# Kernel tuning notes

Hardware: AMD Instinct MI355X
Metric: run time of the kernel (lower is better)

Reference implementation:

```python
import jax, jax.numpy as jnp
import numpy as np

LEAK = 0.01
EPS = 1e-5


def _gcn(x, W, b, src, dst, n):
    # GCNConv: add self-loops, symmetric D^-1/2 (A+I) D^-1/2 normalization
    h = x @ W
    loop = jnp.arange(n)
    s = jnp.concatenate([src, loop])
    d = jnp.concatenate([dst, loop])
    deg = jax.ops.segment_sum(jnp.ones(s.shape[0], h.dtype), d, num_segments=n)
    dinv = jnp.where(deg > 0, jax.lax.rsqrt(deg), 0.0)
    norm = dinv[s] * dinv[d]
    out = jax.ops.segment_sum(h[s] * norm[:, None], d, num_segments=n)
    return out + b


def _sage(x, Wl, bl, Wr, src, dst, n):
    # SAGEConv (mean aggr): lin_l(mean_neigh) + lin_r(x); bias on lin_l
    cnt = jax.ops.segment_sum(jnp.ones(src.shape[0], x.dtype), dst, num_segments=n)
    agg = jax.ops.segment_sum(x[src], dst, num_segments=n) / jnp.maximum(cnt, 1.0)[:, None]
    return agg @ Wl + bl + x @ Wr


def _bn(x, g, b):
    # BatchNorm over node dim, batch statistics (training forward), biased var
    m = x.mean(0)
    v = jnp.mean((x - m) ** 2, axis=0)
    return (x - m) * jax.lax.rsqrt(v + EPS) * g + b


def _lrelu(x):
    return jnp.where(x >= 0, x, LEAK * x)


def setup_inputs() -> dict:
    key = jax.random.key(0)
    ks = jax.random.split(key, 20)
    N, E, F_IN, H, G, L = 50000, 800000, 128, 128, 1000, 1000
    h2, h4, OUT = H // 2, H // 4, 32
    x = jax.random.normal(ks[0], (N, F_IN), dtype=jnp.float32)
    edge_index = jax.random.randint(ks[1], (2, E), 0, N)
    batch = jnp.sort(jax.random.randint(ks[2], (N,), 0, G))
    link_indices = jax.random.randint(ks[3], (2, L), 0, G)
    s = 0.05
    return {
        "x": x, "edge_index": edge_index, "batch": batch,
        "link_indices": link_indices, "num_graphs": G,
        "W1": jax.random.normal(ks[4], (F_IN, H), jnp.float32) * s,
        "b1": jnp.zeros((H,), jnp.float32),
        "g1": jnp.ones((H,), jnp.float32), "be1": jnp.zeros((H,), jnp.float32),
        "Wl2": jax.random.normal(ks[5], (H, h2), jnp.float32) * s,
        "bl2": jnp.zeros((h2,), jnp.float32),
        "Wr2": jax.random.normal(ks[6], (H, h2), jnp.float32) * s,
        "g2": jnp.ones((h2,), jnp.float32), "be2": jnp.zeros((h2,), jnp.float32),
        "W3": jax.random.normal(ks[7], (h2, h4), jnp.float32) * s,
        "b3": jnp.zeros((h4,), jnp.float32),
        "g3": jnp.ones((h4,), jnp.float32), "be3": jnp.zeros((h4,), jnp.float32),
        "W4": jax.random.normal(ks[8], (h4, OUT), jnp.float32) * s,
        "b4": jnp.zeros((OUT,), jnp.float32),
    }


def reference(x, edge_index, batch, link_indices, num_graphs,
              W1, b1, g1, be1, Wl2, bl2, Wr2, g2, be2,
              W3, b3, g3, be3, W4, b4):
    n = x.shape[0]
    src, dst = edge_index[0], edge_index[1]
    h = _lrelu(_bn(_gcn(x, W1, b1, src, dst, n), g1, be1))        # dropout = identity (eval)
    h = _lrelu(_bn(_sage(h, Wl2, bl2, Wr2, src, dst, n), g2, be2))
    h = _lrelu(_bn(_gcn(h, W3, b3, src, dst, n), g3, be3))
    h = _gcn(h, W4, b4, src, dst, n)
    g = jax.ops.segment_sum(h, batch, num_segments=num_graphs)     # global_add_pool
    src_emb = g[link_indices[0]]
    tgt_emb = g[link_indices[1]]
    return jax.nn.sigmoid(jnp.sum(src_emb * tgt_emb, axis=1))
```

## Files before the change

### kernel.cpp

```cpp
#include <hip/hip_runtime.h>
#include <math.h>

#define LEAK 0.01f
#define BNEPS 1e-5f
#define NCH 256
#define NGMAX 1024
#define NSLOT 64

typedef __attribute__((ext_vector_type(8))) short bf16x8;
typedef __attribute__((ext_vector_type(4))) float f32x4;
typedef __attribute__((ext_vector_type(2))) float f32x2;

__device__ inline unsigned bfpack(float a, float b) {
  unsigned ua = __float_as_uint(a);
  unsigned ub = __float_as_uint(b);
  unsigned ra = (ua + 0x7fffu + ((ua >> 16) & 1u)) >> 16;
  unsigned rb = (ub + 0x7fffu + ((ub >> 16) & 1u)) & 0xffff0000u;
  return ra | rb;
}
__device__ inline unsigned short bfround(float a) {
  unsigned ua = __float_as_uint(a);
  return (unsigned short)((ua + 0x7fffu + ((ua >> 16) & 1u)) >> 16);
}
__device__ inline float2 bfunpack(unsigned u) {
  float2 r;
  r.x = __uint_as_float(u << 16);
  r.y = __uint_as_float(u & 0xffff0000u);
  return r;
}
__device__ inline unsigned char f32_to_fp8(float v) {
  int p = __builtin_amdgcn_cvt_pk_fp8_f32(v, v, 0, false);
  return (unsigned char)(p & 0xff);
}

__global__ __launch_bounds__(256) void k_hist(const int* __restrict__ dst,
                                              int* __restrict__ H, int E, int NBK) {
  __shared__ int h[256];
  h[threadIdx.x] = 0;
  __syncthreads();
  int chunk = (E + NCH - 1) / NCH;
  int lo = blockIdx.x * chunk, hi = min(lo + chunk, E);
  for (int e = lo + threadIdx.x; e < hi; e += 256)
    atomicAdd(&h[dst[e] >> 8], 1);
  __syncthreads();
  if (threadIdx.x < NBK) H[threadIdx.x * NCH + blockIdx.x] = h[threadIdx.x];
}

__global__ __launch_bounds__(256) void k_gscan1(const int* __restrict__ in,
                                                int* __restrict__ bsum, int m) {
  int i = blockIdx.x * 256 + threadIdx.x;
  int v = (i < m) ? in[i] : 0;
#pragma unroll
  for (int s = 1; s < 64; s <<= 1) v += __shfl_xor(v, s, 64);
  __shared__ int ws[4];
  if ((threadIdx.x & 63) == 0) ws[threadIdx.x >> 6] = v;
  __syncthreads();
  if (threadIdx.x == 0) bsum[blockIdx.x] = ws[0] + ws[1] + ws[2] + ws[3];
}
__global__ __launch_bounds__(256) void k_gscan2(int* __restrict__ bsum, int NB) {
  __shared__ int lds[256];
  int t = threadIdx.x;
  int v = (t < NB) ? bsum[t] : 0;
  lds[t] = v;
  __syncthreads();
  for (int ofs = 1; ofs < 256; ofs <<= 1) {
    int u = (t >= ofs) ? lds[t - ofs] : 0;
    __syncthreads();
    lds[t] += u;
    __syncthreads();
  }
  if (t < NB) bsum[t] = lds[t] - v;
}
__global__ __launch_bounds__(256) void k_gscan3(const int* __restrict__ in,
                                                const int* __restrict__ boff,
                                                int* __restrict__ out, int m) {
  __shared__ int lds[256];
  int t = threadIdx.x;
  int i = blockIdx.x * 256 + t;
  int v = (i < m) ? in[i] : 0;
  lds[t] = v;
  __syncthreads();
  for (int ofs = 1; ofs < 256; ofs <<= 1) {
    int u = (t >= ofs) ? lds[t - ofs] : 0;
    __syncthreads();
    lds[t] += u;
    __syncthreads();
  }
  if (i < m) out[i] = boff[blockIdx.x] + lds[t] - v;
}

__global__ __launch_bounds__(256) void k_scatter_bkt(
    const int* __restrict__ src, const int* __restrict__ dst,
    const int* __restrict__ O, int* __restrict__ ebuf, int E, int NBK) {
  __shared__ int cur[256];
  if (threadIdx.x < NBK) cur[threadIdx.x] = O[threadIdx.x * NCH + blockIdx.x];
  __syncthreads();
  int chunk = (E + NCH - 1) / NCH;
  int lo = blockIdx.x * chunk, hi = min(lo + chunk, E);
  for (int e = lo + threadIdx.x; e < hi; e += 256) {
    int d = dst[e];
    int pos = atomicAdd(&cur[d >> 8], 1);
    ebuf[pos] = src[e] | ((d & 255) << 24);
  }
}

__global__ __launch_bounds__(256) void k_fill2(
    const int* __restrict__ ebuf, const int* __restrict__ O,
    int* __restrict__ eidx, int* __restrict__ rowptr,
    float* __restrict__ dinv, float* __restrict__ invcnt,
    int E, int n, int NBK) {
  __shared__ int hist[256];
  __shared__ int sc[256];
  __shared__ int cur[256];
  const int b = blockIdx.x;
  const int t = threadIdx.x;
  const int lo = O[b * NCH];
  const int hi = (b + 1 < NBK) ? O[(b + 1) * NCH] : E;
  hist[t] = 0;
  __syncthreads();
  for (int e = lo + t; e < hi; e += 256)
    atomicAdd(&hist[(ebuf[e] >> 24) & 255], 1);
  __syncthreads();
  int v = hist[t];
  sc[t] = v;
  __syncthreads();
  for (int ofs = 1; ofs < 256; ofs <<= 1) {
    int u = (t >= ofs) ? sc[t - ofs] : 0;
    __syncthreads();
    sc[t] += u;
    __syncthreads();
  }
  int excl = sc[t] - v;
  cur[t] = lo + excl;
  int node = b * 256 + t;
  if (node < n) {
    rowptr[node] = lo + excl;
    float d = (float)v;
    dinv[node]   = rsqrtf(d + 1.0f);
    invcnt[node] = 1.0f / fmaxf(d, 1.0f);
  }
  if (node == n || (b == NBK - 1 && t == 255)) rowptr[n] = E;
  __syncthreads();
  for (int e = lo + t; e < hi; e += 256) {
    int p = ebuf[e];
    int pos = atomicAdd(&cur[(p >> 24) & 255], 1);
    eidx[pos] = p & 0xFFFFFF;
  }
}

template<int F, bool FP8, bool GCN, bool ADD, bool STATS, bool POOL>
__global__ __launch_bounds__(256) void k_gather(
    const void* __restrict__ Hn, const unsigned short* __restrict__ Hbf,
    const float* __restrict__ scale,
    const int* __restrict__ rowptr, const int* __restrict__ eidx,
    const float* __restrict__ bias, const float* __restrict__ addf,
    unsigned short* __restrict__ outb,
    float* __restrict__ partials, const int* __restrict__ batch,
    float* __restrict__ gpool, int n) {
  constexpr int COLS = F / 8;
  constexpr int EPI  = 64 / COLS;
  const int wid  = threadIdx.x >> 6;
  const int v    = blockIdx.x * 4 + wid;
  const bool valid = v < n;
  const int lane = threadIdx.x & 63;
  const int col  = lane % COLS;
  const int eo   = lane / COLS;

  const int lo = valid ? rowptr[v] : 0;
  const int hi = valid ? rowptr[v + 1] : 0;
  float a[8] = {0.f,0.f,0.f,0.f,0.f,0.f,0.f,0.f};
  int myE = (lo + lane < hi) ? eidx[lo + lane] : 0;
  for (int base = lo; base < hi; base += 64) {
    int cnt = min(hi - base, 64);
    int nxt = (base + 64 + lane < hi) ? eidx[base + 64 + lane] : 0;
#pragma unroll 4
    for (int t = eo; t < cnt; t += EPI) {
      int s = __shfl(myE, t, 64);
      if constexpr (FP8) {
        uint2 q = *(const uint2*)((const unsigned char*)Hn + (long long)s * F + col * 8);
        f32x2 p0 = __builtin_amdgcn_cvt_pk_f32_fp8(q.x, false);
        f32x2 p1 = __builtin_amdgcn_cvt_pk_f32_fp8(q.x, true);
        f32x2 p2 = __builtin_amdgcn_cvt_pk_f32_fp8(q.y, false);
        f32x2 p3 = __builtin_amdgcn_cvt_pk_f32_fp8(q.y, true);
        a[0]+=p0[0]; a[1]+=p0[1]; a[2]+=p1[0]; a[3]+=p1[1];
        a[4]+=p2[0]; a[5]+=p2[1]; a[6]+=p3[0]; a[7]+=p3[1];
      } else {
        uint4 hv = *(const uint4*)((const unsigned short*)Hn + (long long)s * F + col * 8);
        float2 p0 = bfunpack(hv.x), p1 = bfunpack(hv.y);
        float2 p2 = bfunpack(hv.z), p3 = bfunpack(hv.w);
        a[0]+=p0.x; a[1]+=p0.y; a[2]+=p1.x; a[3]+=p1.y;
        a[4]+=p2.x; a[5]+=p2.y; a[6]+=p3.x; a[7]+=p3.y;
      }
    }
    myE = nxt;
  }
#pragma unroll
  for (int m = COLS; m < 64; m <<= 1) {
#pragma unroll
    for (int j = 0; j < 8; j++) a[j] += __shfl_xor(a[j], m, 64);
  }

  float o[8] = {0.f,0.f,0.f,0.f,0.f,0.f,0.f,0.f};
  if (eo == 0 && valid) {
    float sv = scale[v];
    if constexpr (GCN) {
      uint4 hv = *(const uint4*)&Hbf[(long long)v * F + col * 8];
      float2 p0 = bfunpack(hv.x), p1 = bfunpack(hv.y);
      float2 p2 = bfunpack(hv.z), p3 = bfunpack(hv.w);
      float h[8] = {p0.x,p0.y,p1.x,p1.y,p2.x,p2.y,p3.x,p3.y};
#pragma unroll
      for (int j = 0; j < 8; j++) o[j] = bias[col * 8 + j] + sv * (a[j] + h[j]);
    } else if constexpr (ADD) {
      const float4 t0 = *(const float4*)&addf[(long long)v * F + col * 8];
      const float4 t1 = *(const float4*)&addf[(long long)v * F + col * 8 + 4];
      o[0]=fmaf(sv,a[0],t0.x); o[1]=fmaf(sv,a[1],t0.y);
      o[2]=fmaf(sv,a[2],t0.z); o[3]=fmaf(sv,a[3],t0.w);
      o[4]=fmaf(sv,a[4],t1.x); o[5]=fmaf(sv,a[5],t1.y);
      o[6]=fmaf(sv,a[6],t1.z); o[7]=fmaf(sv,a[7],t1.w);
    } else {
#pragma unroll
      for (int j = 0; j < 8; j++) o[j] = sv * a[j];
    }
    if constexpr (POOL) {
      int g = batch[v];
#pragma unroll
      for (int j = 0; j < 8; j++) atomicAdd(&gpool[(long long)g * F + col * 8 + j], o[j]);
    } else {
      uint4 u;
      u.x = bfpack(o[0], o[1]); u.y = bfpack(o[2], o[3]);
      u.z = bfpack(o[4], o[5]); u.w = bfpack(o[6], o[7]);
      *(uint4*)&outb[(long long)v * F + col * 8] = u;
    }
  }

  if constexpr (STATS) {
    __shared__ float sred[4][2 * F];
    if (eo == 0) {
#pragma unroll
      for (int j = 0; j < 8; j++) {
        sred[wid][col * 8 + j]     = o[j];
        sred[wid][F + col * 8 + j] = o[j] * o[j];
      }
    }
    __syncthreads();
    int t = threadIdx.x;
    if (t < 2 * F) {
      float s = sred[0][t] + sred[1][t] + sred[2][t] + sred[3][t];
      atomicAdd(&partials[(blockIdx.x & (NSLOT - 1)) * 2 * F + t], s);
    }
  }
}

template<int K, int F, bool XBF, bool BNIN, bool F8OUT>
__global__ __launch_bounds__(256) void k_gemm_mfma(
    const void* __restrict__ Xv, const float* __restrict__ W,
    const float* __restrict__ pin, const float* __restrict__ gw,
    const float* __restrict__ bw, float invN,
    const float* __restrict__ prescale,
    unsigned short* __restrict__ Yb, unsigned char* __restrict__ Yf8,
    float* __restrict__ zptr, int zcnt, int n) {
  constexpr int SP  = K + 8;
  constexpr int NCT = F / 16;
  __shared__ unsigned short sX[64 * SP];
  __shared__ unsigned short sWT[F * SP];
  __shared__ float sbn[BNIN ? 2 * K : 1];

  for (int i = blockIdx.x * 256 + threadIdx.x; i < zcnt; i += gridDim.x * 256)
    zptr[i] = 0.f;

  const int row0 = blockIdx.x * 64;
  if constexpr (BNIN) {
    int t = threadIdx.x;
    if (t < K) {
      float s1 = 0.f, s2 = 0.f;
      for (int s = 0; s < NSLOT; s++) {
        s1 += pin[s * 2 * K + t];
        s2 += pin[s * 2 * K + K + t];
      }
      float m   = s1 * invN;
      float var = s2 * invN - m * m;
      float scv = gw[t] * rsqrtf(var + BNEPS);
      sbn[t]     = scv;
      sbn[K + t] = bw[t] - m * scv;
    }
    __syncthreads();
  }
  for (int i = threadIdx.x; i < (K / 2) * F; i += 256) {
    int nn = i % F;
    int kk = (i / F) * 2;
    float w0 = W[(long long)kk * F + nn];
    float w1 = W[(long long)(kk + 1) * F + nn];
    *(unsigned*)&sWT[nn * SP + kk] = bfpack(w0, w1);
  }
  for (int i = threadIdx.x; i < 64 * (K / 8); i += 256) {
    int r = i / (K / 8), k8 = (i % (K / 8)) * 8;
    int gr = row0 + r;
    uint4 u = {0, 0, 0, 0};
    if (gr < n) {
      if constexpr (XBF) {
        const unsigned short* X = (const unsigned short*)Xv;
        uint4 raw = *(const uint4*)&X[(long long)gr * K + k8];
        if constexpr (BNIN) {
          float2 p0 = bfunpack(raw.x), p1 = bfunpack(raw.y);
          float2 p2 = bfunpack(raw.z), p3 = bfunpack(raw.w);
          float y[8] = {p0.x,p0.y,p1.x,p1.y,p2.x,p2.y,p3.x,p3.y};
#pragma unroll
          for (int j = 0; j < 8; j++) {
            float t = fmaf(y[j], sbn[k8 + j], sbn[K + k8 + j]);
            y[j] = (t >= 0.f) ? t : LEAK * t;
          }
          u.x = bfpack(y[0], y[1]); u.y = bfpack(y[2], y[3]);
          u.z = bfpack(y[4], y[5]); u.w = bfpack(y[6], y[7]);
        } else {
          u = raw;
        }
      } else {
        const float* X = (const float*)Xv;
        float4 xa = *(const float4*)&X[(long long)gr * K + k8];
        float4 xb = *(const float4*)&X[(long long)gr * K + k8 + 4];
        u.x = bfpack(xa.x, xa.y); u.y = bfpack(xa.z, xa.w);
        u.z = bfpack(xb.x, xb.y); u.w = bfpack(xb.z, xb.w);
      }
    }
    *(uint4*)&sX[r * SP + k8] = u;
  }
  __syncthreads();

  const int wv   = threadIdx.x >> 6;
  const int lane = threadIdx.x & 63;
  const int l16  = lane & 15;
  const int quad = lane >> 4;
  f32x4 acc[NCT];
#pragma unroll
  for (int c = 0; c < NCT; c++) acc[c] = (f32x4){0.f, 0.f, 0.f, 0.f};

#pragma unroll
  for (int k0 = 0; k0 < K; k0 += 32) {
    bf16x8 af = *(const bf16x8*)&sX[(wv * 16 + l16) * SP + k0 + quad * 8];
#pragma unroll
    for (int c = 0; c < NCT; c++) {
      bf16x8 bfr = *(const bf16x8*)&sWT[(c * 16 + l16) * SP + k0 + quad * 8];
      acc[c] = __builtin_amdgcn_mfma_f32_16x16x32_bf16(af, bfr, acc[c], 0, 0, 0);
    }
  }

  const int rbase = row0 + wv * 16 + quad * 4;
  float ps[4];
#pragma unroll
  for (int rg = 0; rg < 4; rg++) {
    int gr = rbase + rg;
    ps[rg] = (prescale && gr < n) ? prescale[gr] : 1.0f;
  }
#pragma unroll
  for (int c = 0; c < NCT; c++) {
    int col = c * 16 + l16;
#pragma unroll
    for (int rg = 0; rg < 4; rg++) {
      int gr = rbase + rg;
      if (gr < n) {
        float val = acc[c][rg] * ps[rg];
        Yb[(long long)gr * F + col] = bfround(val);
        if constexpr (F8OUT) Yf8[(long long)gr * F + col] = f32_to_fp8(val);
      }
    }
  }
}

__global__ __launch_bounds__(256) void k_gemm_sage_mfma(
    const unsigned short* __restrict__ X, const float* __restrict__ Wl,
    const float* __restrict__ Wr, const float* __restrict__ bl,
    const float* __restrict__ pin, const float* __restrict__ gw,
    const float* __restrict__ bw, float invN,
    unsigned char* __restrict__ t1f8, float* __restrict__ t2,
    float* __restrict__ zptr, int zcnt, int n) {
  constexpr int K = 128, F = 64, SP = K + 8, NCT = F / 16;
  __shared__ unsigned short sX[64 * SP];
  __shared__ unsigned short sWlT[F * SP];
  __shared__ unsigned short sWrT[F * SP];
  __shared__ float sbn[2 * K];

  for (int i = blockIdx.x * 256 + threadIdx.x; i < zcnt; i += gridDim.x * 256)
    zptr[i] = 0.f;

  {
    int t = threadIdx.x;
    if (t < K) {
      float s1 = 0.f, s2 = 0.f;
      for (int s = 0; s < NSLOT; s++) {
        s1 += pin[s * 2 * K + t];
        s2 += pin[s * 2 * K + K + t];
      }
      float m   = s1 * invN;
      float var = s2 * invN - m * m;
      float scv = gw[t] * rsqrtf(var + BNEPS);
      sbn[t]     = scv;
      sbn[K + t] = bw[t] - m * scv;
    }
  }
  __syncthreads();
  const int row0 = blockIdx.x * 64;
  for (int i = threadIdx.x; i < (K / 2) * F; i += 256) {
    int nn = i % F;
    int kk = (i / F) * 2;
    *(unsigned*)&sWlT[nn * SP + kk] =
        bfpack(Wl[(long long)kk * F + nn], Wl[(long long)(kk + 1) * F + nn]);
    *(unsigned*)&sWrT[nn * SP + kk] =
        bfpack(Wr[(long long)kk * F + nn], Wr[(long long)(kk + 1) * F + nn]);
  }
  for (int i = threadIdx.x; i < 64 * (K / 8); i += 256) {
    int r = i / (K / 8), k8 = (i % (K / 8)) * 8;
    int gr = row0 + r;
    uint4 u = {0, 0, 0, 0};
    if (gr < n) {
      uint4 raw = *(const uint4*)&X[(long long)gr * K + k8];
      float2 p0 = bfunpack(raw.x), p1 = bfunpack(raw.y);
      float2 p2 = bfunpack(raw.z), p3 = bfunpack(raw.w);
      float y[8] = {p0.x,p0.y,p1.x,p1.y,p2.x,p2.y,p3.x,p3.y};
#pragma unroll
      for (int j = 0; j < 8; j++) {
        float t = fmaf(y[j], sbn[k8 + j], sbn[K + k8 + j]);
        y[j] = (t >= 0.f) ? t : LEAK * t;
      }
      u.x = bfpack(y[0], y[1]); u.y = bfpack(y[2], y[3]);
      u.z = bfpack(y[4], y[5]); u.w = bfpack(y[6], y[7]);
    }
    *(uint4*)&sX[r * SP + k8] = u;
  }
  __syncthreads();

  const int wv   = threadIdx.x >> 6;
  const int lane = threadIdx.x & 63;
  const int l16  = lane & 15;
  const int quad = lane >> 4;
  f32x4 a1[NCT], a2[NCT];
#pragma unroll
  for (int c = 0; c < NCT; c++) {
    a1[c] = (f32x4){0.f, 0.f, 0.f, 0.f};
    a2[c] = (f32x4){0.f, 0.f, 0.f, 0.f};
  }
#pragma unroll
  for (int k0 = 0; k0 < K; k0 += 32) {
    bf16x8 af = *(const bf16x8*)&sX[(wv * 16 + l16) * SP + k0 + quad * 8];
#pragma unroll
    for (int c = 0; c < NCT; c++) {
      bf16x8 bl8 = *(const bf16x8*)&sWlT[(c * 16 + l16) * SP + k0 + quad * 8];
      bf16x8 br8 = *(const bf16x8*)&sWrT[(c * 16 + l16) * SP + k0 + quad * 8];
      a1[c] = __builtin_amdgcn_mfma_f32_16x16x32_bf16(af, bl8, a1[c], 0, 0, 0);
      a2[c] = __builtin_amdgcn_mfma_f32_16x16x32_bf16(af, br8, a2[c], 0, 0, 0);
    }
  }
  const int rbase = row0 + wv * 16 + quad * 4;
#pragma unroll
  for (int c = 0; c < NCT; c++) {
    int col = c * 16 + l16;
    float blv = bl[col];
#pragma unroll
    for (int rg = 0; rg < 4; rg++) {
      int gr = rbase + rg;
      if (gr < n) {
        t1f8[(long long)gr * F + col] = f32_to_fp8(a1[c][rg]);
        t2[(long long)gr * F + col]   = a2[c][rg] + blv;
      }
    }
  }
}

__global__ void k_link(const float* __restrict__ g, const int* __restrict__ li0,
                       const int* __restrict__ li1, float* __restrict__ out, int L) {
  int i = blockIdx.x * blockDim.x + threadIdx.x;
  if (i >= L) return;
  const float* a = g + (long long)li0[i] * 32;
  const float* b = g + (long long)li1[i] * 32;
  float s = 0.f;
#pragma unroll
  for (int f = 0; f < 32; f++) s = fmaf(a[f], b[f], s);
  out[i] = 1.0f / (1.0f + expf(-s));
}

extern "C" void kernel_launch(void* const* d_in, const int* in_sizes, int n_in,
                              void* d_out, int out_size, void* d_ws, size_t ws_size,
                              hipStream_t stream) {
  const float* x   = (const float*)d_in[0];
  const int* ei    = (const int*)d_in[1];
  const int* batch = (const int*)d_in[2];
  const int* li    = (const int*)d_in[3];
  const float* W1  = (const float*)d_in[5];
  const float* b1  = (const float*)d_in[6];
  const float* g1  = (const float*)d_in[7];
  const float* be1 = (const float*)d_in[8];
  const float* Wl2 = (const float*)d_in[9];
  const float* bl2 = (const float*)d_in[10];
  const float* Wr2 = (const float*)d_in[11];
  const float* g2  = (const float*)d_in[12];
  const float* be2 = (const float*)d_in[13];
  const float* W3  = (const float*)d_in[14];
  const float* b3  = (const float*)d_in[15];
  const float* g3  = (const float*)d_in[16];
  const float* be3 = (const float*)d_in[17];
  const float* W4  = (const float*)d_in[18];
  const float* b4  = (const float*)d_in[19];

  const int n = in_sizes[0] / 128;
  const int E = in_sizes[1] / 2;
  const int L = in_sizes[3] / 2;
  const int* src = ei;
  const int* dst = ei + E;
  const int* li0 = li;
  const int* li1 = li + L;
  const int NBK = (n + 255) / 256;

  char* base = (char*)d_ws;
  size_t off = 0;
  auto alloc = [&](size_t bytes) -> void* {
    void* p = (void*)(base + off);
    off = (off + bytes + 255) & ~(size_t)255;
    return p;
  };
  int*   H      = (int*)alloc((size_t)NBK * NCH * 4);
  int*   O      = (int*)alloc((size_t)NBK * NCH * 4);
  int*   hsum   = (int*)alloc((size_t)1024 * 4);
  int*   ebuf   = (int*)alloc((size_t)E * 4);
  int*   eidx   = (int*)alloc((size_t)E * 4);
  int*   rowptr = (int*)alloc((size_t)(n + 1) * 4);
  float* dinv   = (float*)alloc((size_t)n * 4);
  float* invcnt = (float*)alloc((size_t)n * 4);
  float* partials1 = (float*)alloc((size_t)NSLOT * 256 * 4);
  float* partials2 = (float*)alloc((size_t)NSLOT * 128 * 4);
  float* partials3 = (float*)alloc((size_t)NSLOT * 64 * 4);
  float* gpool  = (float*)alloc((size_t)NGMAX * 32 * 4);
  unsigned short* h1b  = (unsigned short*)alloc((size_t)n * 128 * 2);
  unsigned char*  h1f8 = (unsigned char*)alloc((size_t)n * 128);
  unsigned short* a1b  = (unsigned short*)alloc((size_t)n * 128 * 2);
  unsigned char*  t1f8 = (unsigned char*)alloc((size_t)n * 64);
  float*          t2f  = (float*)alloc((size_t)n * 64 * 4);
  unsigned short* h2b  = (unsigned short*)alloc((size_t)n * 64 * 2);
  unsigned short* h3gb = (unsigned short*)alloc((size_t)n * 32 * 2);
  unsigned short* a3b  = (unsigned short*)alloc((size_t)n * 32 * 2);
  unsigned short* h4b  = (unsigned short*)alloc((size_t)n * 32 * 2);
  (void)ws_size; (void)n_in; (void)out_size;

  const int BT = 256;
  auto cdiv = [](long long a, long long b) { return (int)((a + b - 1) / b); };
  const int GB  = cdiv(n, 4);
  const int GM  = cdiv(n, 64);
  const int MH  = NBK * NCH;
  const int NBH = cdiv(MH, 256);
  const float invN = 1.0f / (float)n;

  k_hist<<<NCH, 256, 0, stream>>>(dst, H, E, NBK);
  k_gscan1<<<NBH, 256, 0, stream>>>(H, hsum, MH);
  k_gscan2<<<1, 256, 0, stream>>>(hsum, NBH);
  k_gscan3<<<NBH, 256, 0, stream>>>(H, hsum, O, MH);
  k_scatter_bkt<<<NCH, 256, 0, stream>>>(src, dst, O, ebuf, E, NBK);
  k_fill2<<<NBK, 256, 0, stream>>>(ebuf, O, eidx, rowptr, dinv, invcnt, E, n, NBK);

  k_gemm_mfma<128,128,false,false,true><<<GM, 256, 0, stream>>>(
      x, W1, nullptr, nullptr, nullptr, 0.f, dinv, h1b, h1f8,
      partials1, NSLOT * 256, n);
  k_gather<128,true,true,false,true,false><<<GB, 256, 0, stream>>>(
      h1f8, h1b, dinv, rowptr, eidx, b1, nullptr, a1b,
      partials1, nullptr, nullptr, n);

  k_gemm_sage_mfma<<<GM, 256, 0, stream>>>(
      a1b, Wl2, Wr2, bl2, partials1, g1, be1, invN, t1f8, t2f,
      partials2, NSLOT * 128, n);
  k_gather<64,true,false,true,true,false><<<GB, 256, 0, stream>>>(
      t1f8, nullptr, invcnt, rowptr, eidx, nullptr, t2f, h2b,
      partials2, nullptr, nullptr, n);

  k_gemm_mfma<64,32,true,true,false><<<GM, 256, 0, stream>>>(
      h2b, W3, partials2, g2, be2, invN, dinv, h3gb, nullptr,
      partials3, NSLOT * 64, n);
  k_gather<32,false,true,false,true,false><<<GB, 256, 0, stream>>>(
      h3gb, h3gb, dinv, rowptr, eidx, b3, nullptr, a3b,
      partials3, nullptr, nullptr, n);

  k_gemm_mfma<32,32,true,true,false><<<GM, 256, 0, stream>>>(
      a3b, W4, partials3, g3, be3, invN, dinv, h4b, nullptr,
      gpool, NGMAX * 32, n);
  k_gather<32,false,true,false,false,true><<<GB, 256, 0, stream>>>(
      h4b, h4b, dinv, rowptr, eidx, b4, nullptr, nullptr,
      nullptr, batch, gpool, n);

  k_link<<<cdiv(L, BT), BT, 0, stream>>>(gpool, li0, li1, (float*)d_out, L);
}
```

Baseline: 357.6 us.

## Map multiple nodes per wave in gather kernels with per-lane edge batches

```diff
diff --git a/kernel.cpp b/kernel.cpp
--- a/kernel.cpp
+++ b/kernel.cpp
@@ -158,61 +158,86 @@
     float* __restrict__ partials, const int* __restrict__ batch,
     float* __restrict__ gpool, int n) {
   constexpr int COLS = F / 8;
-  constexpr int EPI  = 64 / COLS;
-  const int wid  = threadIdx.x >> 6;
-  const int v    = blockIdx.x * 4 + wid;
+  constexpr int GPW  = 64 / COLS;
+  constexpr int NPB  = 4 * GPW;
+  constexpr int K    = 16 / COLS;
+
+  const int tid  = threadIdx.x;
+  const int wave = tid >> 6;
+  const int lane = tid & 63;
+  const int l    = lane % COLS;
+  const int g    = lane / COLS;
+  const int vb   = (int)blockIdx.x * NPB;
+  const int v    = vb + wave * GPW + g;
   const bool valid = v < n;
-  const int lane = threadIdx.x & 63;
-  const int col  = lane % COLS;
-  const int eo   = lane / COLS;
+
+  __shared__ float sred[STATS ? 2 * F : 1];
+  __shared__ float pool[POOL ? NPB * 32 : 1];
+  int gbase = 0;
+  if constexpr (STATS) {
+    if (tid < 2 * F) sred[tid] = 0.f;
+  }
+  if constexpr (POOL) {
+    for (int i = tid; i < NPB * 32; i += 256) pool[i] = 0.f;
+    gbase = batch[min(vb, n - 1)];
+  }
+  if constexpr (STATS || POOL) __syncthreads();
 
   const int lo = valid ? rowptr[v] : 0;
   const int hi = valid ? rowptr[v + 1] : 0;
   float a[8] = {0.f,0.f,0.f,0.f,0.f,0.f,0.f,0.f};
-  int myE = (lo + lane < hi) ? eidx[lo + lane] : 0;
-  for (int base = lo; base < hi; base += 64) {
-    int cnt = min(hi - base, 64);
-    int nxt = (base + 64 + lane < hi) ? eidx[base + 64 + lane] : 0;
-#pragma unroll 4
-    for (int t = eo; t < cnt; t += EPI) {
-      int s = __shfl(myE, t, 64);
-      if constexpr (FP8) {
-        uint2 q = *(const uint2*)((const unsigned char*)Hn + (long long)s * F + col * 8);
-        f32x2 p0 = __builtin_amdgcn_cvt_pk_f32_fp8(q.x, false);
-        f32x2 p1 = __builtin_amdgcn_cvt_pk_f32_fp8(q.x, true);
-        f32x2 p2 = __builtin_amdgcn_cvt_pk_f32_fp8(q.y, false);
-        f32x2 p3 = __builtin_amdgcn_cvt_pk_f32_fp8(q.y, true);
-        a[0]+=p0[0]; a[1]+=p0[1]; a[2]+=p1[0]; a[3]+=p1[1];
-        a[4]+=p2[0]; a[5]+=p2[1]; a[6]+=p3[0]; a[7]+=p3[1];
-      } else {
-        uint4 hv = *(const uint4*)((const unsigned short*)Hn + (long long)s * F + col * 8);
-        float2 p0 = bfunpack(hv.x), p1 = bfunpack(hv.y);
-        float2 p2 = bfunpack(hv.z), p3 = bfunpack(hv.w);
-        a[0]+=p0.x; a[1]+=p0.y; a[2]+=p1.x; a[3]+=p1.y;
-        a[4]+=p2.x; a[5]+=p2.y; a[6]+=p3.x; a[7]+=p3.y;
-      }
-    }
-    myE = nxt;
-  }
-#pragma unroll
-  for (int m = COLS; m < 64; m <<= 1) {
-#pragma unroll
-    for (int j = 0; j < 8; j++) a[j] += __shfl_xor(a[j], m, 64);
+
+  int trips = (hi - lo + 15) >> 4;
+#pragma unroll
+  for (int m = 1; m < 64; m <<= 1) trips = max(trips, __shfl_xor(trips, m, 64));
+
+  for (int bb = 0; bb < trips; bb++) {
+    const int b = lo + bb * 16;
+    int pre[K];
+#pragma unroll
+    for (int kk = 0; kk < K; kk++) {
+      int e = b + l * K + kk;
+      pre[kk] = (e < hi) ? eidx[e] : 0;
+    }
+#pragma unroll
+    for (int j = 0; j < 16; j++) {
+      int s = __shfl(pre[j % K], g * COLS + j / K, 64);
+      if (b + j < hi) {
+        if constexpr (FP8) {
+          uint2 q = *(const uint2*)((const unsigned char*)Hn + (long long)s * F + l * 8);
+          f32x2 p0 = __builtin_amdgcn_cvt_pk_f32_fp8(q.x, false);
+          f32x2 p1 = __builtin_amdgcn_cvt_pk_f32_fp8(q.x, true);
+          f32x2 p2 = __builtin_amdgcn_cvt_pk_f32_fp8(q.y, false);
+          f32x2 p3 = __builtin_amdgcn_cvt_pk_f32_fp8(q.y, true);
+          a[0]+=p0[0]; a[1]+=p0[1]; a[2]+=p1[0]; a[3]+=p1[1];
+          a[4]+=p2[0]; a[5]+=p2[1]; a[6]+=p3[0]; a[7]+=p3[1];
+        } else {
+          uint4 hv = *(const uint4*)((const unsigned short*)Hn + (long long)s * F + l * 8);
+          float2 p0 = bfunpack(hv.x), p1 = bfunpack(hv.y);
+          float2 p2 = bfunpack(hv.z), p3 = bfunpack(hv.w);
+          a[0]+=p0.x; a[1]+=p0.y; a[2]+=p1.x; a[3]+=p1.y;
+          a[4]+=p2.x; a[5]+=p2.y; a[6]+=p3.x; a[7]+=p3.y;
+        }
+      }
+    }
   }
 
   float o[8] = {0.f,0.f,0.f,0.f,0.f,0.f,0.f,0.f};
-  if (eo == 0 && valid) {
+  if (valid) {
     float sv = scale[v];
     if constexpr (GCN) {
-      uint4 hv = *(const uint4*)&Hbf[(long long)v * F + col * 8];
+      uint4 hv = *(const uint4*)&Hbf[(long long)v * F + l * 8];
       float2 p0 = bfunpack(hv.x), p1 = bfunpack(hv.y);
       float2 p2 = bfunpack(hv.z), p3 = bfunpack(hv.w);
       float h[8] = {p0.x,p0.y,p1.x,p1.y,p2.x,p2.y,p3.x,p3.y};
-#pragma unroll
-      for (int j = 0; j < 8; j++) o[j] = bias[col * 8 + j] + sv * (a[j] + h[j]);
+      const float4 b0 = *(const float4*)&bias[l * 8];
+      const float4 b1 = *(const float4*)&bias[l * 8 + 4];
+      float bv[8] = {b0.x,b0.y,b0.z,b0.w,b1.x,b1.y,b1.z,b1.w};
+#pragma unroll
+      for (int j = 0; j < 8; j++) o[j] = bv[j] + sv * (a[j] + h[j]);
     } else if constexpr (ADD) {
-      const float4 t0 = *(const float4*)&addf[(long long)v * F + col * 8];
-      const float4 t1 = *(const float4*)&addf[(long long)v * F + col * 8 + 4];
+      const float4 t0 = *(const float4*)&addf[(long long)v * F + l * 8];
+      const float4 t1 = *(const float4*)&addf[(long long)v * F + l * 8 + 4];
       o[0]=fmaf(sv,a[0],t0.x); o[1]=fmaf(sv,a[1],t0.y);
       o[2]=fmaf(sv,a[2],t0.z); o[3]=fmaf(sv,a[3],t0.w);
       o[4]=fmaf(sv,a[4],t1.x); o[5]=fmaf(sv,a[5],t1.y);
@@ -222,32 +247,36 @@
       for (int j = 0; j < 8; j++) o[j] = sv * a[j];
     }
     if constexpr (POOL) {
-      int g = batch[v];
-#pragma unroll
-      for (int j = 0; j < 8; j++) atomicAdd(&gpool[(long long)g * F + col * 8 + j], o[j]);
+      int gi = batch[v] - gbase;
+#pragma unroll
+      for (int j = 0; j < 8; j++) atomicAdd(&pool[gi * 32 + l * 8 + j], o[j]);
     } else {
       uint4 u;
       u.x = bfpack(o[0], o[1]); u.y = bfpack(o[2], o[3]);
       u.z = bfpack(o[4], o[5]); u.w = bfpack(o[6], o[7]);
-      *(uint4*)&outb[(long long)v * F + col * 8] = u;
+      *(uint4*)&outb[(long long)v * F + l * 8] = u;
     }
   }
 
   if constexpr (STATS) {
-    __shared__ float sred[4][2 * F];
-    if (eo == 0) {
+    if (valid) {
 #pragma unroll
       for (int j = 0; j < 8; j++) {
-        sred[wid][col * 8 + j]     = o[j];
-        sred[wid][F + col * 8 + j] = o[j] * o[j];
-      }
-    }
-    __syncthreads();
-    int t = threadIdx.x;
-    if (t < 2 * F) {
-      float s = sred[0][t] + sred[1][t] + sred[2][t] + sred[3][t];
-      atomicAdd(&partials[(blockIdx.x & (NSLOT - 1)) * 2 * F + t], s);
-    }
+        atomicAdd(&sred[l * 8 + j], o[j]);
+        atomicAdd(&sred[F + l * 8 + j], o[j] * o[j]);
+      }
+    }
+    __syncthreads();
+    if (tid < 2 * F)
+      atomicAdd(&partials[((int)blockIdx.x & (NSLOT - 1)) * 2 * F + tid], sred[tid]);
+  }
+  if constexpr (POOL) {
+    __syncthreads();
+    int vend = min(vb + NPB, n) - 1;
+    int range = batch[vend] - gbase;
+    int total = (range + 1) * 32;
+    for (int t = tid; t < total; t += 256)
+      atomicAdd(&gpool[(long long)gbase * 32 + t], pool[t]);
   }
 }
 
@@ -541,7 +570,6 @@
 
   const int BT = 256;
   auto cdiv = [](long long a, long long b) { return (int)((a + b - 1) / b); };
-  const int GB  = cdiv(n, 4);
   const int GM  = cdiv(n, 64);
   const int MH  = NBK * NCH;
   const int NBH = cdiv(MH, 256);
@@ -557,28 +585,28 @@
   k_gemm_mfma<128,128,false,false,true><<<GM, 256, 0, stream>>>(
       x, W1, nullptr, nullptr, nullptr, 0.f, dinv, h1b, h1f8,
       partials1, NSLOT * 256, n);
-  k_gather<128,true,true,false,true,false><<<GB, 256, 0, stream>>>(
+  k_gather<128,true,true,false,true,false><<<cdiv(n,16), 256, 0, stream>>>(
       h1f8, h1b, dinv, rowptr, eidx, b1, nullptr, a1b,
       partials1, nullptr, nullptr, n);
 
   k_gemm_sage_mfma<<<GM, 256, 0, stream>>>(
       a1b, Wl2, Wr2, bl2, partials1, g1, be1, invN, t1f8, t2f,
       partials2, NSLOT * 128, n);
-  k_gather<64,true,false,true,true,false><<<GB, 256, 0, stream>>>(
+  k_gather<64,true,false,true,true,false><<<cdiv(n,32), 256, 0, stream>>>(
       t1f8, nullptr, invcnt, rowptr, eidx, nullptr, t2f, h2b,
       partials2, nullptr, nullptr, n);
 
   k_gemm_mfma<64,32,true,true,false><<<GM, 256, 0, stream>>>(
       h2b, W3, partials2, g2, be2, invN, dinv, h3gb, nullptr,
       partials3, NSLOT * 64, n);
-  k_gather<32,false,true,false,true,false><<<GB, 256, 0, stream>>>(
+  k_gather<32,false,true,false,true,false><<<cdiv(n,64), 256, 0, stream>>>(
       h3gb, h3gb, dinv, rowptr, eidx, b3, nullptr, a3b,
       partials3, nullptr, nullptr, n);
 
   k_gemm_mfma<32,32,true,true,false><<<GM, 256, 0, stream>>>(
       a3b, W4, partials3, g3, be3, invN, dinv, h4b, nullptr,
       gpool, NGMAX * 32, n);
-  k_gather<32,false,true,false,false,true><<<GB, 256, 0, stream>>>(
+  k_gather<32,false,true,false,false,true><<<cdiv(n,64), 256, 0, stream>>>(
       h4b, h4b, dinv, rowptr, eidx, b4, nullptr, nullptr,
       nullptr, batch, gpool, n);
 
```

Result: slower. 393.0 us (+9.9%).

## Fuse CSR build kernels into one cooperative kernel and use nontemporal gather loads

Applied to the files above, without the earlier changes.

```diff
diff --git a/kernel.cpp b/kernel.cpp
--- a/kernel.cpp
+++ b/kernel.cpp
@@ -1,5 +1,8 @@
 #include <hip/hip_runtime.h>
+#include <hip/hip_cooperative_groups.h>
 #include <math.h>
+
+namespace cg = cooperative_groups;
 
 #define LEAK 0.01f
 #define BNEPS 1e-5f
@@ -10,6 +13,8 @@
 typedef __attribute__((ext_vector_type(8))) short bf16x8;
 typedef __attribute__((ext_vector_type(4))) float f32x4;
 typedef __attribute__((ext_vector_type(2))) float f32x2;
+typedef unsigned int u32x2 __attribute__((ext_vector_type(2)));
+typedef unsigned int u32x4 __attribute__((ext_vector_type(4)));
 
 __device__ inline unsigned bfpack(float a, float b) {
   unsigned ua = __float_as_uint(a);
@@ -33,118 +38,113 @@
   return (unsigned char)(p & 0xff);
 }
 
-__global__ __launch_bounds__(256) void k_hist(const int* __restrict__ dst,
-                                              int* __restrict__ H, int E, int NBK) {
-  __shared__ int h[256];
-  h[threadIdx.x] = 0;
+__global__ __launch_bounds__(256) void k_csr(
+    const int* __restrict__ src, const int* __restrict__ dst,
+    int* __restrict__ H, int* __restrict__ hsum, int* __restrict__ O,
+    int* __restrict__ ebuf, int* __restrict__ eidx, int* __restrict__ rowptr,
+    float* __restrict__ dinv, float* __restrict__ invcnt,
+    int E, int n, int NBK, int NBH, int MH) {
+  cg::grid_group grid = cg::this_grid();
+  __shared__ int s0[256], s1[256], s2[256];
+  const int bid = blockIdx.x;
+  const int t = threadIdx.x;
+  const int chunk = (E + NCH - 1) / NCH;
+
+  s0[t] = 0;
   __syncthreads();
-  int chunk = (E + NCH - 1) / NCH;
-  int lo = blockIdx.x * chunk, hi = min(lo + chunk, E);
-  for (int e = lo + threadIdx.x; e < hi; e += 256)
-    atomicAdd(&h[dst[e] >> 8], 1);
+  {
+    int lo = bid * chunk, hi = min(lo + chunk, E);
+    for (int e = lo + t; e < hi; e += 256) atomicAdd(&s0[dst[e] >> 8], 1);
+  }
   __syncthreads();
-  if (threadIdx.x < NBK) H[threadIdx.x * NCH + blockIdx.x] = h[threadIdx.x];
-}
-
-__global__ __launch_bounds__(256) void k_gscan1(const int* __restrict__ in,
-                                                int* __restrict__ bsum, int m) {
-  int i = blockIdx.x * 256 + threadIdx.x;
-  int v = (i < m) ? in[i] : 0;
-#pragma unroll
-  for (int s = 1; s < 64; s <<= 1) v += __shfl_xor(v, s, 64);
-  __shared__ int ws[4];
-  if ((threadIdx.x & 63) == 0) ws[threadIdx.x >> 6] = v;
+  if (t < NBK) H[t * NCH + bid] = s0[t];
+  grid.sync();
+
+  if (bid < NBH) {
+    int i = bid * 256 + t;
+    int v = (i < MH) ? H[i] : 0;
+#pragma unroll
+    for (int s = 1; s < 64; s <<= 1) v += __shfl_xor(v, s, 64);
+    if ((t & 63) == 0) s1[t >> 6] = v;
+    __syncthreads();
+    if (t == 0) hsum[bid] = s1[0] + s1[1] + s1[2] + s1[3];
+  }
+  grid.sync();
+
+  if (bid == 0) {
+    int v = (t < NBH) ? hsum[t] : 0;
+    s0[t] = v;
+    __syncthreads();
+    for (int ofs = 1; ofs < 256; ofs <<= 1) {
+      int u = (t >= ofs) ? s0[t - ofs] : 0;
+      __syncthreads();
+      s0[t] += u;
+      __syncthreads();
+    }
+    if (t < NBH) hsum[t] = s0[t] - v;
+  }
+  grid.sync();
+
+  if (bid < NBH) {
+    int i = bid * 256 + t;
+    int v = (i < MH) ? H[i] : 0;
+    s0[t] = v;
+    __syncthreads();
+    for (int ofs = 1; ofs < 256; ofs <<= 1) {
+      int u = (t >= ofs) ? s0[t - ofs] : 0;
+      __syncthreads();
+      s0[t] += u;
+      __syncthreads();
+    }
+    if (i < MH) O[i] = hsum[bid] + s0[t] - v;
+  }
+  grid.sync();
+
+  if (t < NBK) s2[t] = O[t * NCH + bid];
   __syncthreads();
-  if (threadIdx.x == 0) bsum[blockIdx.x] = ws[0] + ws[1] + ws[2] + ws[3];
-}
-__global__ __launch_bounds__(256) void k_gscan2(int* __restrict__ bsum, int NB) {
-  __shared__ int lds[256];
-  int t = threadIdx.x;
-  int v = (t < NB) ? bsum[t] : 0;
-  lds[t] = v;
-  __syncthreads();
-  for (int ofs = 1; ofs < 256; ofs <<= 1) {
-    int u = (t >= ofs) ? lds[t - ofs] : 0;
-    __syncthreads();
-    lds[t] += u;
-    __syncthreads();
-  }
-  if (t < NB) bsum[t] = lds[t] - v;
-}
-__global__ __launch_bounds__(256) void k_gscan3(const int* __restrict__ in,
-                                                const int* __restrict__ boff,
-                                                int* __restrict__ out, int m) {
-  __shared__ int lds[256];
-  int t = threadIdx.x;
-  int i = blockIdx.x * 256 + t;
-  int v = (i < m) ? in[i] : 0;
-  lds[t] = v;
-  __syncthreads();
-  for (int ofs = 1; ofs < 256; ofs <<= 1) {
-    int u = (t >= ofs) ? lds[t - ofs] : 0;
-    __syncthreads();
-    lds[t] += u;
-    __syncthreads();
-  }
-  if (i < m) out[i] = boff[blockIdx.x] + lds[t] - v;
-}
-
-__global__ __launch_bounds__(256) void k_scatter_bkt(
-    const int* __restrict__ src, const int* __restrict__ dst,
-    const int* __restrict__ O, int* __restrict__ ebuf, int E, int NBK) {
-  __shared__ int cur[256];
-  if (threadIdx.x < NBK) cur[threadIdx.x] = O[threadIdx.x * NCH + blockIdx.x];
-  __syncthreads();
-  int chunk = (E + NCH - 1) / NCH;
-  int lo = blockIdx.x * chunk, hi = min(lo + chunk, E);
-  for (int e = lo + threadIdx.x; e < hi; e += 256) {
-    int d = dst[e];
-    int pos = atomicAdd(&cur[d >> 8], 1);
-    ebuf[pos] = src[e] | ((d & 255) << 24);
-  }
-}
-
-__global__ __launch_bounds__(256) void k_fill2(
-    const int* __restrict__ ebuf, const int* __restrict__ O,
-    int* __restrict__ eidx, int* __restrict__ rowptr,
-    float* __restrict__ dinv, float* __restrict__ invcnt,
-    int E, int n, int NBK) {
-  __shared__ int hist[256];
-  __shared__ int sc[256];
-  __shared__ int cur[256];
-  const int b = blockIdx.x;
-  const int t = threadIdx.x;
-  const int lo = O[b * NCH];
-  const int hi = (b + 1 < NBK) ? O[(b + 1) * NCH] : E;
-  hist[t] = 0;
-  __syncthreads();
-  for (int e = lo + t; e < hi; e += 256)
-    atomicAdd(&hist[(ebuf[e] >> 24) & 255], 1);
-  __syncthreads();
-  int v = hist[t];
-  sc[t] = v;
-  __syncthreads();
-  for (int ofs = 1; ofs < 256; ofs <<= 1) {
-    int u = (t >= ofs) ? sc[t - ofs] : 0;
-    __syncthreads();
-    sc[t] += u;
-    __syncthreads();
-  }
-  int excl = sc[t] - v;
-  cur[t] = lo + excl;
-  int node = b * 256 + t;
-  if (node < n) {
-    rowptr[node] = lo + excl;
-    float d = (float)v;
-    dinv[node]   = rsqrtf(d + 1.0f);
-    invcnt[node] = 1.0f / fmaxf(d, 1.0f);
-  }
-  if (node == n || (b == NBK - 1 && t == 255)) rowptr[n] = E;
-  __syncthreads();
-  for (int e = lo + t; e < hi; e += 256) {
-    int p = ebuf[e];
-    int pos = atomicAdd(&cur[(p >> 24) & 255], 1);
-    eidx[pos] = p & 0xFFFFFF;
+  {
+    int lo = bid * chunk, hi = min(lo + chunk, E);
+    for (int e = lo + t; e < hi; e += 256) {
+      int d = dst[e];
+      int pos = atomicAdd(&s2[d >> 8], 1);
+      ebuf[pos] = src[e] | ((d & 255) << 24);
+    }
+  }
+  grid.sync();
+
+  if (bid < NBK) {
+    const int lo = O[bid * NCH];
+    const int hi2 = (bid + 1 < NBK) ? O[(bid + 1) * NCH] : E;
+    s0[t] = 0;
+    __syncthreads();
+    for (int e = lo + t; e < hi2; e += 256)
+      atomicAdd(&s0[(ebuf[e] >> 24) & 255], 1);
+    __syncthreads();
+    int v = s0[t];
+    s1[t] = v;
+    __syncthreads();
+    for (int ofs = 1; ofs < 256; ofs <<= 1) {
+      int u = (t >= ofs) ? s1[t - ofs] : 0;
+      __syncthreads();
+      s1[t] += u;
+      __syncthreads();
+    }
+    int excl = s1[t] - v;
+    s2[t] = lo + excl;
+    int node = bid * 256 + t;
+    if (node < n) {
+      rowptr[node] = lo + excl;
+      float d = (float)v;
+      dinv[node]   = rsqrtf(d + 1.0f);
+      invcnt[node] = 1.0f / fmaxf(d, 1.0f);
+    }
+    if (node == n || (bid == NBK - 1 && t == 255)) rowptr[n] = E;
+    __syncthreads();
+    for (int e = lo + t; e < hi2; e += 256) {
+      int p = ebuf[e];
+      int pos = atomicAdd(&s2[(p >> 24) & 255], 1);
+      eidx[pos] = p & 0xFFFFFF;
+    }
   }
 }
 
@@ -177,17 +177,19 @@
     for (int t = eo; t < cnt; t += EPI) {
       int s = __shfl(myE, t, 64);
       if constexpr (FP8) {
-        uint2 q = *(const uint2*)((const unsigned char*)Hn + (long long)s * F + col * 8);
-        f32x2 p0 = __builtin_amdgcn_cvt_pk_f32_fp8(q.x, false);
-        f32x2 p1 = __builtin_amdgcn_cvt_pk_f32_fp8(q.x, true);
-        f32x2 p2 = __builtin_amdgcn_cvt_pk_f32_fp8(q.y, false);
-        f32x2 p3 = __builtin_amdgcn_cvt_pk_f32_fp8(q.y, true);
+        u32x2 q = __builtin_nontemporal_load(
+            (const u32x2*)((const unsigned char*)Hn + (long long)s * F + col * 8));
+        f32x2 p0 = __builtin_amdgcn_cvt_pk_f32_fp8(q[0], false);
+        f32x2 p1 = __builtin_amdgcn_cvt_pk_f32_fp8(q[0], true);
+        f32x2 p2 = __builtin_amdgcn_cvt_pk_f32_fp8(q[1], false);
+        f32x2 p3 = __builtin_amdgcn_cvt_pk_f32_fp8(q[1], true);
         a[0]+=p0[0]; a[1]+=p0[1]; a[2]+=p1[0]; a[3]+=p1[1];
         a[4]+=p2[0]; a[5]+=p2[1]; a[6]+=p3[0]; a[7]+=p3[1];
       } else {
-        uint4 hv = *(const uint4*)((const unsigned short*)Hn + (long long)s * F + col * 8);
-        float2 p0 = bfunpack(hv.x), p1 = bfunpack(hv.y);
-        float2 p2 = bfunpack(hv.z), p3 = bfunpack(hv.w);
+        u32x4 hv = __builtin_nontemporal_load(
+            (const u32x4*)((const unsigned short*)Hn + (long long)s * F + col * 8));
+        float2 p0 = bfunpack(hv[0]), p1 = bfunpack(hv[1]);
+        float2 p2 = bfunpack(hv[2]), p3 = bfunpack(hv[3]);
         a[0]+=p0.x; a[1]+=p0.y; a[2]+=p1.x; a[3]+=p1.y;
         a[4]+=p2.x; a[5]+=p2.y; a[6]+=p3.x; a[7]+=p3.y;
       }
@@ -246,7 +248,7 @@
     int t = threadIdx.x;
     if (t < 2 * F) {
       float s = sred[0][t] + sred[1][t] + sred[2][t] + sred[3][t];
-      atomicAdd(&partials[(blockIdx.x & (NSLOT - 1)) * 2 * F + t], s);
+      atomicAdd(&partials[((int)blockIdx.x & (NSLOT - 1)) * 2 * F + t], s);
     }
   }
 }
@@ -547,12 +549,15 @@
   const int NBH = cdiv(MH, 256);
   const float invN = 1.0f / (float)n;
 
-  k_hist<<<NCH, 256, 0, stream>>>(dst, H, E, NBK);
-  k_gscan1<<<NBH, 256, 0, stream>>>(H, hsum, MH);
-  k_gscan2<<<1, 256, 0, stream>>>(hsum, NBH);
-  k_gscan3<<<NBH, 256, 0, stream>>>(H, hsum, O, MH);
-  k_scatter_bkt<<<NCH, 256, 0, stream>>>(src, dst, O, ebuf, E, NBK);
-  k_fill2<<<NBK, 256, 0, stream>>>(ebuf, O, eidx, rowptr, dinv, invcnt, E, n, NBK);
+  {
+    int E_ = E, n_ = n, NBK_ = NBK, NBH_ = NBH, MH_ = MH;
+    void* kargs[] = {
+      (void*)&src, (void*)&dst, (void*)&H, (void*)&hsum, (void*)&O,
+      (void*)&ebuf, (void*)&eidx, (void*)&rowptr, (void*)&dinv, (void*)&invcnt,
+      (void*)&E_, (void*)&n_, (void*)&NBK_, (void*)&NBH_, (void*)&MH_
+    };
+    hipLaunchCooperativeKernel((void*)k_csr, dim3(NCH), dim3(256), kargs, 0, stream);
+  }
 
   k_gemm_mfma<128,128,false,false,true><<<GM, 256, 0, stream>>>(
       x, W1, nullptr, nullptr, nullptr, 0.f, dinv, h1b, h1f8,
```

After: 552.4 us. 54.5% more time.
